# Kernel tuning notes

Hardware: AMD Instinct MI355X
Metric: run time of the kernel (lower is better)

## Reference

```python
import jax, jax.numpy as jnp
import numpy as np

N, C, K, KEIG, B, NG, H = 32768, 128, 5, 128, 64, 512, 4
E = 524288
EPS = 1e-5


def setup_inputs() -> dict:
    key = jax.random.key(0)
    ks = iter(jax.random.split(key, 40))
    def nrm(shape, scale):
        return jax.random.normal(next(ks), shape, jnp.float32) * scale
    s = 1.0 / np.sqrt(C)
    return dict(
        x=nrm((N, C), 1.0),
        U=nrm((N, KEIG), 1.0 / np.sqrt(N)),
        Lambda=jax.random.uniform(next(ks), (KEIG,), jnp.float32, 0.0, 2.0),
        lambda_max=jnp.full((1,), 2.0, jnp.float32),
        w_spa1=nrm((C, C), s), b_spa1=jnp.zeros((C,), jnp.float32),
        w_spa2=nrm((C, C), s), b_spa2=jnp.zeros((C,), jnp.float32),
        w_spe1=nrm((C, C), s), b_spe1=jnp.zeros((C,), jnp.float32),
        w_spe2=nrm((C, C), s), b_spe2=jnp.zeros((C,), jnp.float32),
        cheb_w=nrm((K, C, C), s), cheb_b=jnp.zeros((C,), jnp.float32),
        gamma=jnp.ones((1,), jnp.float32),
        w_proj=nrm((C, C), s),
        w_qkv=nrm((C, 3 * C), s), b_qkv=jnp.zeros((3 * C,), jnp.float32),
        w_out=nrm((C, C), s), b_out=jnp.zeros((C,), jnp.float32),
        mlp_w1=nrm((C, 2 * C), s), mlp_b1=jnp.zeros((2 * C,), jnp.float32),
        mlp_w2=nrm((2 * C, C), 1.0 / np.sqrt(2 * C)), mlp_b2=jnp.zeros((C,), jnp.float32),
        bn1_w=jnp.ones((C,), jnp.float32), bn1_b=jnp.zeros((C,), jnp.float32),
        bn2_w=jnp.ones((C,), jnp.float32), bn2_b=jnp.zeros((C,), jnp.float32),
        bn3_w=jnp.ones((C,), jnp.float32), bn3_b=jnp.zeros((C,), jnp.float32),
        edge_index=jax.random.randint(next(ks), (2, E), 0, N, jnp.int64) if jax.config.jax_enable_x64 else jax.random.randint(next(ks), (2, E), 0, N, jnp.int32),
        batch=jnp.repeat(jnp.arange(B), NG),  # 64 graphs of 512 nodes each
    )


def _mlp2(h, w1, b1, w2, b2):
    return jnp.maximum(h @ w1 + b1, 0.0) @ w2 + b2


def _bn(h, w, b):
    # train-mode BatchNorm1d over node dim (biased variance), GPSConv default norm
    mu = h.mean(0)
    var = jnp.mean((h - mu) ** 2, 0)
    return (h - mu) * jax.lax.rsqrt(var + EPS) * w + b


def _cheb(x, src, dst, lam, Ws, bias):
    # L_hat = (2/lambda_max) * (I - D^{-1/2} A D^{-1/2}) - I ; sym normalization
    deg = jax.ops.segment_sum(jnp.ones_like(src, x.dtype), src, num_segments=N)
    dis = jnp.where(deg > 0, 1.0 / jnp.sqrt(deg), 0.0)
    w = dis[src] * dis[dst]  # [E]
    scale = 2.0 / lam
    def lhat(v):
        agg = jax.ops.segment_sum(w[:, None] * v[src], dst, num_segments=N)
        return (scale - 1.0) * v - scale * agg
    Tx0 = x
    out = Tx0 @ Ws[0]
    Tx1 = lhat(Tx0)
    out = out + Tx1 @ Ws[1]
    for k in range(2, K):
        Tx2 = 2.0 * lhat(Tx1) - Tx0
        out = out + Tx2 @ Ws[k]
        Tx0, Tx1 = Tx1, Tx2
    return out + bias


def _mha(xd, w_qkv, b_qkv, w_out, b_out):
    Bq, n, _ = xd.shape
    dh = C // H
    qkv = xd @ w_qkv + b_qkv  # [B,n,3C]
    q, k, v = jnp.split(qkv, 3, axis=-1)
    heads = lambda t: t.reshape(Bq, n, H, dh).transpose(0, 2, 1, 3)
    q, k, v = heads(q), heads(k), heads(v)
    a = jax.nn.softmax(jnp.einsum('bhqd,bhkd->bhqk', q, k) / np.sqrt(dh), axis=-1)
    o = jnp.einsum('bhqk,bhkd->bhqd', a, v).transpose(0, 2, 1, 3).reshape(Bq, n, C)
    return o @ w_out + b_out


def reference(x, U, Lambda, lambda_max,
              w_spa1, b_spa1, w_spa2, b_spa2,
              w_spe1, b_spe1, w_spe2, b_spe2,
              cheb_w, cheb_b, gamma, w_proj,
              w_qkv, b_qkv, w_out, b_out,
              mlp_w1, mlp_b1, mlp_w2, mlp_b2,
              bn1_w, bn1_b, bn2_w, bn2_b, bn3_w, bn3_b,
              edge_index, batch):
    src, dst = edge_index[0], edge_index[1]
    lam = lambda_max[0]
    # ---- SpectralLocalNN (GPSConv local conv branch) ----
    x_sp = _mlp2(x, w_spa1, b_spa1, w_spa2, b_spa2)
    out_local = _cheb(x_sp, src, dst, lam, cheb_w, cheb_b)
    x_spec = _mlp2(x, w_spe1, b_spe1, w_spe2, b_spe2)
    h_proj = x_spec @ w_proj
    s_lam = jnp.exp(-gamma[0] * Lambda ** 2)  # [k_eig]
    out_spectral = U @ (s_lam[:, None] * (U.T @ h_proj))
    h1 = _bn(out_local + out_spectral + x, bn1_w, bn1_b)
    # ---- global attention branch (equal-size graphs -> dense reshape) ----
    xd = x.reshape(B, NG, C)
    h2 = _mha(xd, w_qkv, b_qkv, w_out, b_out).reshape(N, C)
    h2 = _bn(h2 + x, bn2_w, bn2_b)
    # ---- combine + MLP ----
    out = h1 + h2
    out = out + _mlp2(out, mlp_w1, mlp_b1, mlp_w2, mlp_b2)
    return _bn(out, bn3_w, bn3_b)
```

## Files before the change

### kernel.cpp

```cpp
#include <hip/hip_runtime.h>

typedef short bf16x8 __attribute__((ext_vector_type(8)));
typedef short bf16x4 __attribute__((ext_vector_type(4)));
typedef float f32x4 __attribute__((ext_vector_type(4)));

#define DEVI __device__ __forceinline__

constexpr int N   = 32768;
constexpr int C   = 128;
constexpr int E   = 524288;
constexpr float EPSV = 1e-5f;
constexpr int UT_BLOCKS = 128;
constexpr int HB  = 64;
constexpr int EPB = E / HB;
constexpr float QSCALE = 0.17677669529663687f * 1.4426950408889634f;

DEVI float bf2f(ushort u){ return __uint_as_float(((uint)u) << 16); }
DEVI ushort f2bf(float f){
  uint u = __float_as_uint(f);
  return (ushort)((u + 0x7fffu + ((u >> 16) & 1u)) >> 16);
}
DEVI uint cvtpk(float lo, float hi){
  uint r;
  asm("v_cvt_pk_bf16_f32 %0, %1, %2" : "=v"(r) : "v"(lo), "v"(hi));
  return r;
}
DEVI float fexp2(float x){
  float r;
  asm("v_exp_f32 %0, %1" : "=v"(r) : "v"(x));
  return r;
}
DEVI float sane(float v){ if (!(v == v)) return 0.f; return fminf(fmaxf(v, -1e30f), 1e30f); }
DEVI bool mode_fp32(const uint* lmraw){ return (lmraw[0] & 0xffffu) == 0u; }

constexpr int CSZ[28] = {128,1,16384,128,16384,128,16384,128,16384,128,81920,128,
                         1,16384,49152,384,16384,128,32768,256,32768,128,
                         128,128,128,128,128,128};
constexpr int COF[28] = {0,128,192,16576,16704,33088,33216,49600,49728,66112,
                         66240,148160,148288,148352,164736,213888,214272,230656,
                         230784,263552,263808,296576,296704,296832,296960,297088,
                         297216,297344};
constexpr int CAN_SMALL_TOTAL = 297472;

constexpr int WT_SPA1 = 0;
constexpr int WT_SPA2 = 16384;
constexpr int WT_SPE1 = 32768;
constexpr int WT_SPE2 = 49152;
constexpr int WT_PROJ = 65536;
constexpr int WT_CHEB = 81920;
constexpr int WT_QKV  = 163840;
constexpr int WT_WOUT = 212992;
constexpr int WT_MLP1 = 229376;
constexpr int WT_MLP2 = 262144;
constexpr int WT_TOTAL = 294912;

struct CvtArgs { const void* src[28]; };

DEVI ushort cvt_elem(const void* p, int j, bool f32){
  return f32 ? f2bf(((const float*)p)[j]) : ((const ushort*)p)[j];
}

__global__ __launch_bounds__(256) void prep_all(CvtArgs a,
    const void* __restrict__ xs, const void* __restrict__ Us,
    ushort* __restrict__ canx, ushort* __restrict__ canu,
    ushort* __restrict__ cs, ushort* __restrict__ wt,
    int* __restrict__ zp, const uint* __restrict__ lmraw)
{
  bool f32 = mode_fp32(lmraw);
  int b = blockIdx.x, tid = threadIdx.x;
  if (b < 8192) {
    size_t e = ((size_t)b * 256 + tid) * 4;
    bool isU = e >= (size_t)N * C;
    size_t off = isU ? e - (size_t)N * C : e;
    const void* src = isU ? Us : xs;
    ushort* dst = isU ? canu : canx;
    ushort4 o;
    if (f32) {
      float4 v = *(const float4*)((const float*)src + off);
      o.x = f2bf(v.x); o.y = f2bf(v.y); o.z = f2bf(v.z); o.w = f2bf(v.w);
    } else {
      o = *(const ushort4*)((const ushort*)src + off);
    }
    *(ushort4*)(dst + off) = o;
  } else if (b < 9354) {
    int idx = (b - 8192) * 256 + tid;
    #pragma unroll 1
    for (int s = 0; s < 28; s++) {
      if (idx < CSZ[s]) { cs[COF[s] + idx] = cvt_elem(a.src[s], idx, f32); return; }
      idx -= CSZ[s];
    }
  } else if (b < 10506) {
    int i = (b - 9354) * 256 + tid;
    if (i < 81920) {
      int m = i >> 14, r = i & 16383; int k = r >> 7, n = r & 127;
      const void* src = m==0?a.src[2] : m==1?a.src[4] : m==2?a.src[6] : m==3?a.src[8] : a.src[13];
      wt[m*16384 + n*128 + k] = cvt_elem(src, r, f32);
    } else if (i < 163840) {
      int j = i - 81920; int m = j >> 14, r = j & 16383; int k = r >> 7, n = r & 127;
      wt[WT_CHEB + n*640 + m*128 + k] = cvt_elem(a.src[10], j, f32);
    } else if (i < 212992) {
      int j = i - 163840; int k = j / 384, n = j % 384;
      wt[WT_QKV + n*128 + k] = cvt_elem(a.src[14], j, f32);
    } else if (i < 229376) {
      int j = i - 212992; int k = j >> 7, n = j & 127;
      wt[WT_WOUT + n*128 + k] = cvt_elem(a.src[16], j, f32);
    } else if (i < 262144) {
      int j = i - 229376; int k = j >> 8, n = j & 255;
      wt[WT_MLP1 + n*128 + k] = cvt_elem(a.src[18], j, f32);
    } else if (i < WT_TOTAL) {
      int j = i - 262144; int k = j >> 7, n = j & 127;
      wt[WT_MLP2 + n*256 + k] = cvt_elem(a.src[20], j, f32);
    }
  } else {
    int i = (b - 10506) * 256 + tid;
    if (i < 6144) zp[i] = 0;
  }
}

__global__ __launch_bounds__(1024) void hist_lds(const int* __restrict__ ei,
    int* __restrict__ cei, ushort* __restrict__ part)
{
  __shared__ uint hist[N / 2];
  int t = threadIdx.x;
  int b = blockIdx.x;
  bool i64 = ((ei[1] | ei[3] | ei[5] | ei[7]) == 0);
  size_t j0 = (size_t)b * EPB;
  #pragma unroll
  for (int i = t; i < N / 2; i += 1024) hist[i] = 0u;
  __syncthreads();
  for (int k = t; k < EPB; k += 1024) {
    size_t j = j0 + k;
    int v = (i64 ? ei[2 * j] : ei[j]) & (N - 1);
    cei[j] = v;
    atomicAdd(&hist[v >> 1], 1u << ((v & 1) * 16));
  }
  __syncthreads();
  uint* po = (uint*)(part + (size_t)b * N);
  for (int i = t; i < N / 2; i += 1024) po[i] = hist[i];
}

__global__ __launch_bounds__(256) void reduce_cnt(const ushort* __restrict__ part,
    int* __restrict__ cdt, float* __restrict__ dis)
{
  int d = blockIdx.x * 256 + threadIdx.x;
  int s = 0, tt = 0;
  #pragma unroll 8
  for (int b = 0; b < HB; b++) s  += part[(size_t)b * N + d];
  #pragma unroll 8
  for (int b = 0; b < HB; b++) tt += part[(size_t)(HB + b) * N + d];
  cdt[d] = tt;
  dis[d] = s > 0 ? rsqrtf((float)s) : 0.f;
}

__global__ __launch_bounds__(1024) void scan_kernel(const int* __restrict__ cnt,
                                                    int* __restrict__ row_ptr)
{
  __shared__ int sums[1024];
  int t = threadIdx.x;
  int loc[32]; int s = 0;
  int base = t * 32;
  #pragma unroll
  for (int i = 0; i < 32; i++) { loc[i] = s; s += cnt[base + i]; }
  sums[t] = s;
  __syncthreads();
  for (int off = 1; off < 1024; off <<= 1) {
    int v = (t >= off) ? sums[t - off] : 0;
    __syncthreads();
    sums[t] += v;
    __syncthreads();
  }
  int pre = (t == 0) ? 0 : sums[t - 1];
  #pragma unroll
  for (int i = 0; i < 32; i++) row_ptr[base + i] = pre + loc[i];
}

__global__ __launch_bounds__(256) void off_kernel(const int* __restrict__ rp,
    const ushort* __restrict__ part, int* __restrict__ off2)
{
  int d = blockIdx.x * 256 + threadIdx.x;
  int run = rp[d];
  #pragma unroll 8
  for (int b = 0; b < HB; b++) {
    off2[(size_t)b * N + d] = run;
    run += part[(size_t)(HB + b) * N + d];
  }
}

__global__ __launch_bounds__(1024) void edge_scatter(const int* __restrict__ cei,
    const int* __restrict__ off2, const float* __restrict__ dis,
    int2* __restrict__ ep)
{
  __shared__ int base[N];
  int t = threadIdx.x;
  int b = blockIdx.x;
  for (int i = t; i < N; i += 1024) base[i] = off2[(size_t)b * N + i];
  __syncthreads();
  size_t e0 = (size_t)b * EPB;
  for (int k = t; k < EPB; k += 1024) {
    size_t e = e0 + k;
    int s = cei[e], d = cei[e + E];
    int slot = atomicAdd(&base[d], 1);
    int2 v; v.x = s; v.y = __float_as_int(dis[s] * dis[d]);
    ep[slot] = v;
  }
}

template<int K, int COLS, bool RELU, int OMODE, bool BIAS, bool RES, int ASTR, int OSTR, bool QSC, bool STATS>
__global__ __launch_bounds__(256) void gemm_lds(
    const ushort* __restrict__ A, const ushort* __restrict__ WT,
    const ushort* __restrict__ bias, const ushort* __restrict__ res,
    void* __restrict__ outp, float* __restrict__ gstats)
{
  constexpr int NSEG = COLS / 128;
  constexpr int NKC = K / 128;
  constexpr int BP = 136;
  __shared__ ushort Bs[128 * BP];
  __shared__ float ls[STATS ? 256 : 1];
  int tid = threadIdx.x;
  int lane = tid & 63, wave = tid >> 6;
  int quad = lane >> 4, l16 = lane & 15;
  int seg = (NSEG > 1) ? (blockIdx.x % NSEG) : 0;
  int rb  = (NSEG > 1) ? (blockIdx.x / NSEG) : blockIdx.x;
  int row0 = rb * 64 + wave * 16;
  const ushort* wseg = WT + (size_t)(seg * 128) * K;

  f32x4 acc[8];
  #pragma unroll
  for (int nt = 0; nt < 8; nt++) acc[nt] = (f32x4){0.f, 0.f, 0.f, 0.f};

  for (int kc = 0; kc < NKC; kc++) {
    if (kc) __syncthreads();
    #pragma unroll
    for (int i = tid; i < 2048; i += 256) {
      int col = i >> 4, ko = (i & 15) * 8;
      *(bf16x8*)&Bs[col * BP + ko] =
          *(const bf16x8*)(wseg + (size_t)col * K + kc * 128 + ko);
    }
    __syncthreads();
    bf16x8 a[4];
    const ushort* ap = A + (size_t)(row0 + l16) * ASTR + kc * 128 + quad * 8;
    #pragma unroll
    for (int kk = 0; kk < 4; kk++) a[kk] = *(const bf16x8*)(ap + kk * 32);
    #pragma unroll
    for (int kk = 0; kk < 4; kk++) {
      #pragma unroll
      for (int nt = 0; nt < 8; nt++) {
        bf16x8 b = *(const bf16x8*)(&Bs[(nt * 16 + l16) * BP + kk * 32 + quad * 8]);
        acc[nt] = __builtin_amdgcn_mfma_f32_16x16x32_bf16(a[kk], b, acc[nt], 0, 0, 0);
      }
    }
  }

  if (STATS) {
    if (tid < 256) ls[tid] = 0.f;
    __syncthreads();
  }

  #pragma unroll
  for (int nt = 0; nt < 8; nt++) {
    int col = seg * 128 + nt * 16 + l16;
    float bv = 0.f;
    if (BIAS) bv = bf2f(bias[col]);
    float cs_ = 0.f, cs2 = 0.f;
    #pragma unroll
    for (int r = 0; r < 4; r++) {
      int row = row0 + quad * 4 + r;
      size_t oi = (size_t)row * OSTR + col;
      float v = acc[nt][r] + bv;
      if (RES) v += bf2f(res[(size_t)row * COLS + col]);
      if (RELU) v = fmaxf(v, 0.f);
      if (QSC && col < 128) v *= QSCALE;
      float nv;
      if (OMODE == 0)      { ((ushort*)outp)[oi] = f2bf(v); nv = v; }
      else if (OMODE == 1) { ((float*)outp)[oi] = v; nv = v; }
      else                 { float* fo = (float*)outp + oi; nv = *fo + v; *fo = nv; }
      if (STATS) { float sv = sane(nv); cs_ += sv; cs2 += sv * sv; }
    }
    if (STATS) { atomicAdd(&ls[col], cs_); atomicAdd(&ls[128 + col], cs2); }
  }

  if (STATS) {
    __syncthreads();
    float* gs = gstats + (blockIdx.x & 7) * 256;
    if (tid < 128) {
      atomicAdd(&gs[tid], ls[tid]);
      atomicAdd(&gs[128 + tid], ls[128 + tid]);
    }
  }
}

__global__ __launch_bounds__(256) void gemm_qkv(
    const ushort* __restrict__ A, const ushort* __restrict__ WT,
    const ushort* __restrict__ bias, ushort* __restrict__ outp)
{
  constexpr int BP = 136;
  __shared__ ushort Bs[128 * BP];
  int tid = threadIdx.x;
  int lane = tid & 63, wave = tid >> 6;
  int quad = lane >> 4, l16 = lane & 15;
  int row0 = blockIdx.x * 64 + wave * 16;
  bf16x8 a[4];
  {
    const ushort* ap = A + (size_t)(row0 + l16) * 128 + quad * 8;
    #pragma unroll
    for (int kk = 0; kk < 4; kk++) a[kk] = *(const bf16x8*)(ap + kk * 32);
  }

  #pragma unroll 1
  for (int seg = 0; seg < 3; seg++) {
    if (seg) __syncthreads();
    for (int i = tid; i < 2048; i += 256) {
      int col = i >> 4, ko = (i & 15) * 8;
      *(bf16x8*)&Bs[col * BP + ko] =
          *(const bf16x8*)(WT + (size_t)(seg * 128 + col) * 128 + ko);
    }
    __syncthreads();
    f32x4 acc[8];
    #pragma unroll
    for (int nt = 0; nt < 8; nt++) acc[nt] = (f32x4){0.f, 0.f, 0.f, 0.f};
    #pragma unroll
    for (int kk = 0; kk < 4; kk++)
      #pragma unroll
      for (int nt = 0; nt < 8; nt++) {
        bf16x8 b = *(const bf16x8*)(&Bs[(nt * 16 + l16) * BP + kk * 32 + quad * 8]);
        acc[nt] = __builtin_amdgcn_mfma_f32_16x16x32_bf16(a[kk], b, acc[nt], 0, 0, 0);
      }
    #pragma unroll
    for (int nt = 0; nt < 8; nt++) {
      int col = seg * 128 + nt * 16 + l16;
      float bv = bf2f(bias[col]);
      #pragma unroll
      for (int r = 0; r < 4; r++) {
        float v = acc[nt][r] + bv;
        if (seg == 0) v *= QSCALE;
        outp[(size_t)(row0 + quad * 4 + r) * 384 + col] = f2bf(v);
      }
    }
  }
}

template<bool THIRD, int OSTR>
__global__ __launch_bounds__(256) void gemm_chain(
    const ushort* __restrict__ A,
    const ushort* __restrict__ W1, const ushort* __restrict__ B1,
    const ushort* __restrict__ W2, const ushort* __restrict__ B2,
    const ushort* __restrict__ W3,
    ushort* __restrict__ outp)
{
  constexpr int BP = 136;
  __shared__ ushort Bs[128 * BP];
  __shared__ ushort Ts[64 * BP];
  int tid = threadIdx.x;
  int lane = tid & 63, wave = tid >> 6;
  int quad = lane >> 4, l16 = lane & 15;
  int row0 = blockIdx.x * 64 + wave * 16;
  int lw = wave * 16;

  for (int i = tid; i < 2048; i += 256) {
    int col = i >> 4, ko = (i & 15) * 8;
    *(bf16x8*)&Bs[col * BP + ko] = *(const bf16x8*)(W1 + (size_t)col * 128 + ko);
  }
  __syncthreads();
  bf16x8 a[4];
  {
    const ushort* ap = A + (size_t)(row0 + l16) * 128 + quad * 8;
    #pragma unroll
    for (int kk = 0; kk < 4; kk++) a[kk] = *(const bf16x8*)(ap + kk * 32);
  }
  f32x4 acc[8];
  #pragma unroll
  for (int nt = 0; nt < 8; nt++) acc[nt] = (f32x4){0.f, 0.f, 0.f, 0.f};
  #pragma unroll
  for (int kk = 0; kk < 4; kk++)
    #pragma unroll
    for (int nt = 0; nt < 8; nt++) {
      bf16x8 b = *(const bf16x8*)(&Bs[(nt * 16 + l16) * BP + kk * 32 + quad * 8]);
      acc[nt] = __builtin_amdgcn_mfma_f32_16x16x32_bf16(a[kk], b, acc[nt], 0, 0, 0);
    }
  #pragma unroll
  for (int nt = 0; nt < 8; nt++) {
    int col = nt * 16 + l16;
    float bv = bf2f(B1[col]);
    #pragma unroll
    for (int r = 0; r < 4; r++)
      Ts[(lw + quad * 4 + r) * BP + col] = f2bf(fmaxf(acc[nt][r] + bv, 0.f));
  }
  __syncthreads();

  for (int i = tid; i < 2048; i += 256) {
    int col = i >> 4, ko = (i & 15) * 8;
    *(bf16x8*)&Bs[col * BP + ko] = *(const bf16x8*)(W2 + (size_t)col * 128 + ko);
  }
  #pragma unroll
  for (int kk = 0; kk < 4; kk++)
    a[kk] = *(const bf16x8*)(&Ts[(lw + l16) * BP + kk * 32 + quad * 8]);
  __syncthreads();
  #pragma unroll
  for (int nt = 0; nt < 8; nt++) acc[nt] = (f32x4){0.f, 0.f, 0.f, 0.f};
  #pragma unroll
  for (int kk = 0; kk < 4; kk++)
    #pragma unroll
    for (int nt = 0; nt < 8; nt++) {
      bf16x8 b = *(const bf16x8*)(&Bs[(nt * 16 + l16) * BP + kk * 32 + quad * 8]);
      acc[nt] = __builtin_amdgcn_mfma_f32_16x16x32_bf16(a[kk], b, acc[nt], 0, 0, 0);
    }

  if (!THIRD) {
    #pragma unroll
    for (int nt = 0; nt < 8; nt++) {
      int col = nt * 16 + l16;
      float bv = bf2f(B2[col]);
      #pragma unroll
      for (int r = 0; r < 4; r++)
        outp[(size_t)(row0 + quad * 4 + r) * OSTR + col] = f2bf(acc[nt][r] + bv);
    }
    return;
  }

  __syncthreads();
  #pragma unroll
  for (int nt = 0; nt < 8; nt++) {
    int col = nt * 16 + l16;
    float bv = bf2f(B2[col]);
    #pragma unroll
    for (int r = 0; r < 4; r++)
      Ts[(lw + quad * 4 + r) * BP + col] = f2bf(acc[nt][r] + bv);
  }
  __syncthreads();
  for (int i = tid; i < 2048; i += 256) {
    int col = i >> 4, ko = (i & 15) * 8;
    *(bf16x8*)&Bs[col * BP + ko] = *(const bf16x8*)(W3 + (size_t)col * 128 + ko);
  }
  #pragma unroll
  for (int kk = 0; kk < 4; kk++)
    a[kk] = *(const bf16x8*)(&Ts[(lw + l16) * BP + kk * 32 + quad * 8]);
  __syncthreads();
  #pragma unroll
  for (int nt = 0; nt < 8; nt++) acc[nt] = (f32x4){0.f, 0.f, 0.f, 0.f};
  #pragma unroll
  for (int kk = 0; kk < 4; kk++)
    #pragma unroll
    for (int nt = 0; nt < 8; nt++) {
      bf16x8 b = *(const bf16x8*)(&Bs[(nt * 16 + l16) * BP + kk * 32 + quad * 8]);
      acc[nt] = __builtin_amdgcn_mfma_f32_16x16x32_bf16(a[kk], b, acc[nt], 0, 0, 0);
    }
  #pragma unroll
  for (int nt = 0; nt < 8; nt++) {
    int col = nt * 16 + l16;
    #pragma unroll
    for (int r = 0; r < 4; r++)
      outp[(size_t)(row0 + quad * 4 + r) * OSTR + col] = f2bf(acc[nt][r]);
  }
}

__global__ __launch_bounds__(256) void gemm_mlp(
    const ushort* __restrict__ A,
    const ushort* __restrict__ W1, const ushort* __restrict__ B1,
    const ushort* __restrict__ W2, const ushort* __restrict__ B2,
    const ushort* __restrict__ res, float* __restrict__ outp,
    float* __restrict__ gstats)
{
  constexpr int BP = 136;
  constexpr int HP = 264;
  __shared__ ushort Bs[128 * BP];
  __shared__ ushort Hs[64 * HP];
  __shared__ float ls[256];
  int tid = threadIdx.x;
  int lane = tid & 63, wave = tid >> 6;
  int quad = lane >> 4, l16 = lane & 15;
  int row0 = blockIdx.x * 64 + wave * 16;
  int lw = wave * 16;

  bf16x8 a[4];
  {
    const ushort* ap = A + (size_t)(row0 + l16) * 128 + quad * 8;
    #pragma unroll
    for (int kk = 0; kk < 4; kk++) a[kk] = *(const bf16x8*)(ap + kk * 32);
  }

  for (int seg = 0; seg < 2; seg++) {
    if (seg) __syncthreads();
    for (int i = tid; i < 2048; i += 256) {
      int col = i >> 4, ko = (i & 15) * 8;
      *(bf16x8*)&Bs[col * BP + ko] =
          *(const bf16x8*)(W1 + (size_t)(seg * 128 + col) * 128 + ko);
    }
    __syncthreads();
    f32x4 acc[8];
    #pragma unroll
    for (int nt = 0; nt < 8; nt++) acc[nt] = (f32x4){0.f, 0.f, 0.f, 0.f};
    #pragma unroll
    for (int kk = 0; kk < 4; kk++)
      #pragma unroll
      for (int nt = 0; nt < 8; nt++) {
        bf16x8 b = *(const bf16x8*)(&Bs[(nt * 16 + l16) * BP + kk * 32 + quad * 8]);
        acc[nt] = __builtin_amdgcn_mfma_f32_16x16x32_bf16(a[kk], b, acc[nt], 0, 0, 0);
      }
    #pragma unroll
    for (int nt = 0; nt < 8; nt++) {
      int col = seg * 128 + nt * 16 + l16;
      float bv = bf2f(B1[col]);
      #pragma unroll
      for (int r = 0; r < 4; r++)
        Hs[(lw + quad * 4 + r) * HP + col] = f2bf(fmaxf(acc[nt][r] + bv, 0.f));
    }
  }
  __syncthreads();
  if (tid < 256) ls[tid] = 0.f;

  f32x4 acc2[8];
  #pragma unroll
  for (int nt = 0; nt < 8; nt++) acc2[nt] = (f32x4){0.f, 0.f, 0.f, 0.f};
  for (int kc = 0; kc < 2; kc++) {
    if (kc) __syncthreads();
    for (int i = tid; i < 2048; i += 256) {
      int col = i >> 4, ko = (i & 15) * 8;
      *(bf16x8*)&Bs[col * BP + ko] =
          *(const bf16x8*)(W2 + (size_t)col * 256 + kc * 128 + ko);
    }
    bf16x8 a2[4];
    #pragma unroll
    for (int kk = 0; kk < 4; kk++)
      a2[kk] = *(const bf16x8*)(&Hs[(lw + l16) * HP + kc * 128 + kk * 32 + quad * 8]);
    __syncthreads();
    #pragma unroll
    for (int kk = 0; kk < 4; kk++)
      #pragma unroll
      for (int nt = 0; nt < 8; nt++) {
        bf16x8 b = *(const bf16x8*)(&Bs[(nt * 16 + l16) * BP + kk * 32 + quad * 8]);
        acc2[nt] = __builtin_amdgcn_mfma_f32_16x16x32_bf16(a2[kk], b, acc2[nt], 0, 0, 0);
      }
  }

  #pragma unroll
  for (int nt = 0; nt < 8; nt++) {
    int col = nt * 16 + l16;
    float bv = bf2f(B2[col]);
    float cs_ = 0.f, cs2 = 0.f;
    #pragma unroll
    for (int r = 0; r < 4; r++) {
      int row = row0 + quad * 4 + r;
      float v = acc2[nt][r] + bv + bf2f(res[(size_t)row * 128 + col]);
      outp[(size_t)row * 128 + col] = v;
      float sv = sane(v); cs_ += sv; cs2 += sv * sv;
    }
    atomicAdd(&ls[col], cs_); atomicAdd(&ls[128 + col], cs2);
  }
  __syncthreads();
  float* gs = gstats + (blockIdx.x & 7) * 256;
  if (tid < 128) {
    atomicAdd(&gs[tid], ls[tid]);
    atomicAdd(&gs[128 + tid], ls[128 + tid]);
  }
}

__global__ __launch_bounds__(256) void spmm_cheb(
    const int* __restrict__ row_ptr, const int2* __restrict__ ep,
    const ushort* __restrict__ v,
    const ushort* __restrict__ txprev, ushort* __restrict__ txout,
    const ushort* __restrict__ lambda_max, int first, int str)
{
  int wave = threadIdx.x >> 6, lane = threadIdx.x & 63;
  int sub = lane >> 4, l16 = lane & 15;
  int d = blockIdx.x * 4 + wave;
  float lm = bf2f(lambda_max[0]);
  float scale = 2.f / lm;
  if (!(scale == scale) || fabsf(scale) > 1e6f) scale = 1.f;
  int beg = row_ptr[d];
  int end = (d == N - 1) ? E : row_ptr[d + 1];
  float acc[8] = {0.f,0.f,0.f,0.f,0.f,0.f,0.f,0.f};
  int j0 = beg + sub;
  int2 eA = ep[j0 < end ? j0 : 0];
  int2 eB = ep[(j0 + 4) < end ? (j0 + 4) : 0];
  bf16x8 vA = *(const bf16x8*)(v + (size_t)(eA.x & (N - 1)) * str + l16 * 8);
  for (int jb = beg; jb < end; jb += 4) {
    int jc = jb + 8 + sub;
    int2 eC = ep[jc < end ? jc : 0];
    bf16x8 vB = *(const bf16x8*)(v + (size_t)(eB.x & (N - 1)) * str + l16 * 8);
    bool ok = (jb + sub) < end;
    float w = ok ? __int_as_float(eA.y) : 0.f;
    #pragma unroll
    for (int i = 0; i < 8; i++) acc[i] += w * bf2f((ushort)vA[i]);
    eA = eB; eB = eC; vA = vB;
  }
  #pragma unroll
  for (int i = 0; i < 8; i++) {
    acc[i] += __shfl_xor(acc[i], 16);
    acc[i] += __shfl_xor(acc[i], 32);
  }
  if (sub == 0) {
    bf16x8 vd = *(const bf16x8*)(v + (size_t)d * str + l16 * 8);
    bf16x8 tp;
    if (!first) tp = *(const bf16x8*)(txprev + (size_t)d * str + l16 * 8);
    bf16x8 ov;
    #pragma unroll
    for (int i = 0; i < 8; i++) {
      float r = (scale - 1.f) * bf2f((ushort)vd[i]) - scale * acc[i];
      if (!first) r = 2.f * r - bf2f((ushort)tp[i]);
      ov[i] = (short)f2bf(r);
    }
    *(bf16x8*)(txout + (size_t)d * str + l16 * 8) = ov;
  }
}

__global__ __launch_bounds__(256) void ut_mfma(const ushort* __restrict__ U,
    const ushort* __restrict__ hp, float* __restrict__ parts)
{
  constexpr int RP = 40;
  __shared__ ushort Ut[128 * RP];
  __shared__ ushort Ht[128 * RP];
  int t = threadIdx.x;
  int lane = t & 63, wave = t >> 6;
  int quad = lane >> 4, l16 = lane & 15;

  f32x4 acc[2][8];
  #pragma unroll
  for (int a = 0; a < 2; a++)
    #pragma unroll
    for (int ct = 0; ct < 8; ct++) acc[a][ct] = (f32x4){0.f, 0.f, 0.f, 0.f};

  for (int ch = 0; ch < 8; ch++) {
    int n0 = blockIdx.x * 256 + ch * 32;
    __syncthreads();
    for (int i = t; i < 2048; i += 256) {
      int r2 = i >> 7, c = i & 127;
      uint u0 = U [(size_t)(n0 + r2 * 2) * 128 + c];
      uint u1 = U [(size_t)(n0 + r2 * 2 + 1) * 128 + c];
      *(uint*)&Ut[c * RP + r2 * 2] = (u0 & 0xffffu) | (u1 << 16);
      uint h0 = hp[(size_t)(n0 + r2 * 2) * 128 + c];
      uint h1 = hp[(size_t)(n0 + r2 * 2 + 1) * 128 + c];
      *(uint*)&Ht[c * RP + r2 * 2] = (h0 & 0xffffu) | (h1 << 16);
    }
    __syncthreads();
    bf16x8 bfr[8];
    #pragma unroll
    for (int ct = 0; ct < 8; ct++)
      bfr[ct] = *(const bf16x8*)(&Ht[(ct * 16 + l16) * RP + quad * 8]);
    #pragma unroll
    for (int a = 0; a < 2; a++) {
      int kt = wave * 2 + a;
      bf16x8 af = *(const bf16x8*)(&Ut[(kt * 16 + l16) * RP + quad * 8]);
      #pragma unroll
      for (int ct = 0; ct < 8; ct++)
        acc[a][ct] = __builtin_amdgcn_mfma_f32_16x16x32_bf16(af, bfr[ct], acc[a][ct], 0, 0, 0);
    }
  }

  float* po = parts + (size_t)blockIdx.x * 16384;
  #pragma unroll
  for (int a = 0; a < 2; a++) {
    int kt = wave * 2 + a;
    #pragma unroll
    for (int ct = 0; ct < 8; ct++)
      #pragma unroll
      for (int r = 0; r < 4; r++)
        po[(kt * 16 + quad * 4 + r) * 128 + ct * 16 + l16] = acc[a][ct][r];
  }
}

__global__ __launch_bounds__(256) void reduce_mt(const float* __restrict__ parts,
    const ushort* __restrict__ Lambda, const ushort* __restrict__ gamma,
    ushort* __restrict__ MT)
{
  int e = blockIdx.x * 256 + threadIdx.x;
  int keig = e >> 7, c = e & 127;
  float s = 0.f;
  for (int p = 0; p < UT_BLOCKS; p++) s += parts[(size_t)p * 16384 + e];
  float g = bf2f(gamma[0]);
  float lam = bf2f(Lambda[keig]);
  float sl = __expf(-g * lam * lam);
  MT[c * 128 + keig] = f2bf(sl * s);
}

__global__ __launch_bounds__(256) void bn_apply(const float* __restrict__ h,
    const float* __restrict__ st, const ushort* __restrict__ gw,
    const ushort* __restrict__ gb, const ushort* __restrict__ add,
    void* __restrict__ out, const uint* __restrict__ lmraw, int final_out)
{
  __shared__ float sk[128], sb[128];
  int tid = threadIdx.x;
  if (tid < 128) {
    float s = 0.f, s2 = 0.f;
    #pragma unroll
    for (int rr = 0; rr < 8; rr++) {
      s  += st[rr * 256 + tid];
      s2 += st[rr * 256 + 128 + tid];
    }
    float mu  = s * (1.f / 32768.f);
    float var = fmaxf(s2 * (1.f / 32768.f) - mu * mu, 0.f);
    float k = rsqrtf(var + EPSV) * bf2f(gw[tid]);
    sk[tid] = k;
    sb[tid] = bf2f(gb[tid]) - mu * k;
  }
  __syncthreads();
  size_t e = ((size_t)blockIdx.x * 256 + tid) * 4;
  int c0 = (int)(e & 127);
  float4 hv = *(const float4*)(h + e);
  float xv[4] = {sane(hv.x), sane(hv.y), sane(hv.z), sane(hv.w)};
  float addv[4] = {0.f, 0.f, 0.f, 0.f};
  if (add) {
    ushort4 av = *(const ushort4*)(add + e);
    addv[0] = bf2f(av.x); addv[1] = bf2f(av.y);
    addv[2] = bf2f(av.z); addv[3] = bf2f(av.w);
  }
  float r[4];
  #pragma unroll
  for (int j = 0; j < 4; j++) {
    int c = c0 + j;
    r[j] = xv[j] * sk[c] + sb[c] + addv[j];
  }
  if (final_out && mode_fp32(lmraw)) {
    float4 o4; o4.x = r[0]; o4.y = r[1]; o4.z = r[2]; o4.w = r[3];
    *(float4*)((float*)out + e) = o4;
  } else {
    ushort4 o;
    o.x = f2bf(r[0]); o.y = f2bf(r[1]); o.z = f2bf(r[2]); o.w = f2bf(r[3]);
    *(ushort4*)((ushort*)out + e) = o;
  }
}

__global__ __launch_bounds__(256) void bn12_apply(
    const float* __restrict__ ha, const float* __restrict__ hb,
    const float* __restrict__ st1, const float* __restrict__ st2,
    const ushort* __restrict__ w1, const ushort* __restrict__ b1,
    const ushort* __restrict__ w2, const ushort* __restrict__ b2,
    ushort* __restrict__ comb)
{
  __shared__ float k1[128], o1[128], k2[128], o2[128];
  int tid = threadIdx.x;
  if (tid < 128) {
    float s = 0.f, s2 = 0.f, t = 0.f, t2 = 0.f;
    #pragma unroll
    for (int rr = 0; rr < 8; rr++) {
      s  += st1[rr * 256 + tid];  s2 += st1[rr * 256 + 128 + tid];
      t  += st2[rr * 256 + tid];  t2 += st2[rr * 256 + 128 + tid];
    }
    float mu  = s * (1.f / 32768.f);
    float var = fmaxf(s2 * (1.f / 32768.f) - mu * mu, 0.f);
    float k = rsqrtf(var + EPSV) * bf2f(w1[tid]);
    k1[tid] = k; o1[tid] = bf2f(b1[tid]) - mu * k;
    mu  = t * (1.f / 32768.f);
    var = fmaxf(t2 * (1.f / 32768.f) - mu * mu, 0.f);
    k = rsqrtf(var + EPSV) * bf2f(w2[tid]);
    k2[tid] = k; o2[tid] = bf2f(b2[tid]) - mu * k;
  }
  __syncthreads();
  size_t e = ((size_t)blockIdx.x * 256 + tid) * 4;
  int c0 = (int)(e & 127);
  float4 av = *(const float4*)(ha + e);
  float4 bv = *(const float4*)(hb + e);
  float xa[4] = {sane(av.x), sane(av.y), sane(av.z), sane(av.w)};
  float xb[4] = {sane(bv.x), sane(bv.y), sane(bv.z), sane(bv.w)};
  ushort4 o;
  ushort r_[4];
  #pragma unroll
  for (int j = 0; j < 4; j++) {
    int c = c0 + j;
    float h1v = bf2f(f2bf(xa[j] * k1[c] + o1[c]));
    r_[j] = f2bf(xb[j] * k2[c] + o2[c] + h1v);
  }
  o.x = r_[0]; o.y = r_[1]; o.z = r_[2]; o.w = r_[3];
  *(ushort4*)(comb + e) = o;
}

__global__ __launch_bounds__(512) void attn_mfma(const ushort* __restrict__ qkv,
                                                 ushort* __restrict__ attn)
{
  constexpr int VP = 516;
  constexpr int KP = 40;
  __shared__ ushort Kt[512 * KP];
  __shared__ ushort Vt[32 * VP];
  int b = blockIdx.x;
  int g = b >> 3, hh = (b >> 1) & 3, half = b & 1;
  int lane = threadIdx.x & 63, wave = threadIdx.x >> 6;
  int quad = lane >> 4, l16 = lane & 15;
  const ushort* base = qkv + (size_t)g * 512 * 384;

  for (int i = threadIdx.x; i < 512 * 4; i += 512) {
    int key = i >> 2, c8 = (i & 3) * 8;
    *(bf16x8*)&Kt[key * KP + c8] =
        *(const bf16x8*)(base + (size_t)key * 384 + 128 + hh * 32 + c8);
  }
  for (int i = threadIdx.x; i < 256 * 8; i += 512) {
    int kp = i >> 3, d4 = (i & 7) * 4;
    const ushort* va = base + (size_t)(2 * kp) * 384 + 256 + hh * 32 + d4;
    ushort4 a = *(const ushort4*)va;
    ushort4 c = *(const ushort4*)(va + 384);
    *(uint*)&Vt[(d4 + 0) * VP + 2 * kp] = (uint)a.x | ((uint)c.x << 16);
    *(uint*)&Vt[(d4 + 1) * VP + 2 * kp] = (uint)a.y | ((uint)c.y << 16);
    *(uint*)&Vt[(d4 + 2) * VP + 2 * kp] = (uint)a.z | ((uint)c.z << 16);
    *(uint*)&Vt[(d4 + 3) * VP + 2 * kp] = (uint)a.w | ((uint)c.w << 16);
  }
  __syncthreads();

  int q0 = half * 256 + wave * 32;
  bf16x8 qf[2];
  #pragma unroll
  for (int i = 0; i < 2; i++)
    qf[i] = *(const bf16x8*)(base + (size_t)(q0 + i * 16 + l16) * 384 + hh * 32 + quad * 8);

  f32x4 O[2][2];
  #pragma unroll
  for (int dt = 0; dt < 2; dt++)
    #pragma unroll
    for (int i = 0; i < 2; i++) O[dt][i] = (f32x4){0.f, 0.f, 0.f, 0.f};
  float lsum[2] = {0.f, 0.f};

  union PU { uint u[4]; bf16x8 v; };
  union VU { uint2 a[2]; bf16x8 v; };

  for (int kt2 = 0; kt2 < 16; kt2++) {
    int k0 = kt2 * 32;
    bf16x8 kfA = *(const bf16x8*)&Kt[(k0 + l16) * KP + quad * 8];
    bf16x8 kfB = *(const bf16x8*)&Kt[(k0 + 16 + l16) * KP + quad * 8];
    PU pw[2];
    #pragma unroll
    for (int i = 0; i < 2; i++) {
      f32x4 sA = __builtin_amdgcn_mfma_f32_16x16x32_bf16(kfA, qf[i], (f32x4){0.f,0.f,0.f,0.f}, 0, 0, 0);
      f32x4 sB = __builtin_amdgcn_mfma_f32_16x16x32_bf16(kfB, qf[i], (f32x4){0.f,0.f,0.f,0.f}, 0, 0, 0);
      float p0 = fexp2(fminf(sA[0], 86.5f));
      float p1 = fexp2(fminf(sA[1], 86.5f));
      float p2 = fexp2(fminf(sA[2], 86.5f));
      float p3 = fexp2(fminf(sA[3], 86.5f));
      float p4 = fexp2(fminf(sB[0], 86.5f));
      float p5 = fexp2(fminf(sB[1], 86.5f));
      float p6 = fexp2(fminf(sB[2], 86.5f));
      float p7 = fexp2(fminf(sB[3], 86.5f));
      lsum[i] += ((p0 + p1) + (p2 + p3)) + ((p4 + p5) + (p6 + p7));
      pw[i].u[0] = cvtpk(p0, p1); pw[i].u[1] = cvtpk(p2, p3);
      pw[i].u[2] = cvtpk(p4, p5); pw[i].u[3] = cvtpk(p6, p7);
    }
    #pragma unroll
    for (int dt = 0; dt < 2; dt++) {
      int drow = (dt * 16 + l16) * VP;
      VU vu;
      vu.a[0] = *(const uint2*)&Vt[drow + k0 + quad * 4];
      vu.a[1] = *(const uint2*)&Vt[drow + k0 + 16 + quad * 4];
      #pragma unroll
      for (int i = 0; i < 2; i++)
        O[dt][i] = __builtin_amdgcn_mfma_f32_16x16x32_bf16(vu.v, pw[i].v, O[dt][i], 0, 0, 0);
    }
  }

  #pragma unroll
  for (int i = 0; i < 2; i++) {
    float l = lsum[i];
    l += __shfl_xor(l, 16);
    l += __shfl_xor(l, 32);
    lsum[i] = 1.f / l;
  }

  #pragma unroll
  for (int i = 0; i < 2; i++) {
    size_t node = (size_t)g * 512 + q0 + i * 16 + l16;
    #pragma unroll
    for (int dt = 0; dt < 2; dt++) {
      uint2 o;
      o.x = cvtpk(O[dt][i][0] * lsum[i], O[dt][i][1] * lsum[i]);
      o.y = cvtpk(O[dt][i][2] * lsum[i], O[dt][i][3] * lsum[i]);
      *(uint2*)(attn + node * 128 + hh * 32 + dt * 16 + quad * 4) = o;
    }
  }
}

constexpr size_t KB = 1024;
constexpr size_t MB = 1048576;
constexpr size_t OFF_WT    = 0;
constexpr size_t OFF_CDT   = 576 * KB;
constexpr size_t OFF_RP    = 704 * KB;
constexpr size_t OFF_DIS   = 832 * KB;
constexpr size_t OFF_MT    = 960 * KB;
constexpr size_t OFF_STATS = 1024 * KB;
constexpr size_t OFF_CEI   = 6  * MB;
constexpr size_t OFF_EP    = 10 * MB;
constexpr size_t OFF_CANX  = 14 * MB;
constexpr size_t OFF_CANU  = 22 * MB;
constexpr size_t OFF_CANS  = 30 * MB;
constexpr size_t OFF_F1    = 31 * MB;
constexpr size_t OFF_HPROJ = 39 * MB;
constexpr size_t OFF_TBIG  = 47 * MB;
constexpr size_t OFF_PARTH = OFF_TBIG;
constexpr size_t OFF_OFF2  = OFF_TBIG + 8 * MB;
constexpr size_t OFF_F1B   = 71 * MB;
constexpr size_t OFF_PARTS = 87 * MB;

extern "C" void kernel_launch(void* const* d_in, const int* in_sizes, int n_in,
                              void* d_out, int out_size, void* d_ws, size_t ws_size,
                              hipStream_t stream) {
  (void)in_sizes; (void)n_in; (void)out_size; (void)ws_size;
  const uint* lmraw = (const uint*)d_in[3];
  const int*  ei    = (const int*)d_in[30];

  char* W = (char*)d_ws;
  ushort* wt    = (ushort*)(W + OFF_WT);
  int*    cdt   = (int*)(W + OFF_CDT);
  int*    rp    = (int*)(W + OFF_RP);
  float*  dis   = (float*)(W + OFF_DIS);
  ushort* MT    = (ushort*)(W + OFF_MT);
  float*  stats = (float*)(W + OFF_STATS);
  int*    cei   = (int*)(W + OFF_CEI);
  int2*   ep    = (int2*)(W + OFF_EP);
  ushort* part  = (ushort*)(W + OFF_PARTH);
  int*    off2  = (int*)(W + OFF_OFF2);
  ushort* canx  = (ushort*)(W + OFF_CANX);
  ushort* canu  = (ushort*)(W + OFF_CANU);
  ushort* cs    = (ushort*)(W + OFF_CANS);
  float*  F1    = (float*)(W + OFF_F1);
  float*  F1B   = (float*)(W + OFF_F1B);
  ushort* hproj = (ushort*)(W + OFF_HPROJ);
  ushort* Tbig  = (ushort*)(W + OFF_TBIG);
  ushort* qkvb  = (ushort*)(W + OFF_TBIG);
  float*  parts = (float*)(W + OFF_PARTS);
  ushort* attnb = (ushort*)(W + OFF_PARTS);
  ushort* comb  = (ushort*)(W + OFF_CANX);

  const ushort* cLambda = cs + COF[0];
  const ushort* cLmx    = cs + COF[1];
  const ushort* cBspa1  = cs + COF[3];
  const ushort* cBspa2  = cs + COF[5];
  const ushort* cBspe1  = cs + COF[7];
  const ushort* cBspe2  = cs + COF[9];
  const ushort* cChebB  = cs + COF[11];
  const ushort* cGam    = cs + COF[12];
  const ushort* cBqkv   = cs + COF[15];
  const ushort* cBout   = cs + COF[17];
  const ushort* cMb1    = cs + COF[19];
  const ushort* cMb2    = cs + COF[21];
  const ushort* cBn1w   = cs + COF[22];
  const ushort* cBn1b   = cs + COF[23];
  const ushort* cBn2w   = cs + COF[24];
  const ushort* cBn2b   = cs + COF[25];
  const ushort* cBn3w   = cs + COF[26];
  const ushort* cBn3b   = cs + COF[27];

  const ushort* NUL = nullptr;
  float* NULF = nullptr;

  CvtArgs ca;
  ca.src[0]  = d_in[2];  ca.src[1]  = d_in[3];  ca.src[2]  = d_in[4];
  ca.src[3]  = d_in[5];  ca.src[4]  = d_in[6];  ca.src[5]  = d_in[7];
  ca.src[6]  = d_in[8];  ca.src[7]  = d_in[9];  ca.src[8]  = d_in[10];
  ca.src[9]  = d_in[11]; ca.src[10] = d_in[12]; ca.src[11] = d_in[13];
  ca.src[12] = d_in[14]; ca.src[13] = d_in[15]; ca.src[14] = d_in[16];
  ca.src[15] = d_in[17]; ca.src[16] = d_in[18]; ca.src[17] = d_in[19];
  ca.src[18] = d_in[20]; ca.src[19] = d_in[21]; ca.src[20] = d_in[22];
  ca.src[21] = d_in[23]; ca.src[22] = d_in[24]; ca.src[23] = d_in[25];
  ca.src[24] = d_in[26]; ca.src[25] = d_in[27]; ca.src[26] = d_in[28];
  ca.src[27] = d_in[29];
  prep_all<<<10530, 256, 0, stream>>>(ca, d_in[0], d_in[1], canx, canu, cs, wt,
                                      (int*)(W + OFF_STATS), lmraw);

  hist_lds<<<2 * HB, 1024, 0, stream>>>(ei, cei, part);
  reduce_cnt<<<N / 256, 256, 0, stream>>>(part, cdt, dis);
  scan_kernel<<<1, 1024, 0, stream>>>(cdt, rp);
  off_kernel<<<N / 256, 256, 0, stream>>>(rp, part, off2);
  edge_scatter<<<HB, 1024, 0, stream>>>(cei, off2, dis, ep);

  dim3 g1(512), bb(256);
  gemm_chain<false, 640><<<g1, bb, 0, stream>>>(canx, wt + WT_SPA1, cBspa1,
      wt + WT_SPA2, cBspa2, NUL, Tbig);
  gemm_chain<true, 128><<<g1, bb, 0, stream>>>(canx, wt + WT_SPE1, cBspe1,
      wt + WT_SPE2, cBspe2, wt + WT_PROJ, hproj);

  ut_mfma<<<UT_BLOCKS, 256, 0, stream>>>(canu, hproj, parts);
  reduce_mt<<<64, 256, 0, stream>>>(parts, cLambda, cGam, MT);

  spmm_cheb<<<N / 4, 256, 0, stream>>>(rp, ep, Tbig,       NUL,        Tbig + 128, cLmx, 1, 640);
  spmm_cheb<<<N / 4, 256, 0, stream>>>(rp, ep, Tbig + 128, Tbig,       Tbig + 256, cLmx, 0, 640);
  spmm_cheb<<<N / 4, 256, 0, stream>>>(rp, ep, Tbig + 256, Tbig + 128, Tbig + 384, cLmx, 0, 640);
  spmm_cheb<<<N / 4, 256, 0, stream>>>(rp, ep, Tbig + 384, Tbig + 256, Tbig + 512, cLmx, 0, 640);
  gemm_lds<640,128,false,1,true ,false,640,128,false,false><<<g1, bb, 0, stream>>>(Tbig, wt + WT_CHEB, cChebB, NUL, F1, NULF);

  gemm_lds<128,128,false,2,false,true ,128,128,false,true ><<<g1, bb, 0, stream>>>(canu, MT, NUL, canx, F1, stats);

  gemm_qkv<<<g1, bb, 0, stream>>>(canx, wt + WT_QKV, cBqkv, qkvb);
  attn_mfma<<<512, 512, 0, stream>>>(qkvb, attnb);
  gemm_lds<128,128,false,1,true ,true ,128,128,false,true ><<<g1, bb, 0, stream>>>(attnb, wt + WT_WOUT, cBout, canx, F1B, stats + 2048);

  bn12_apply<<<(N * C) / 1024, 256, 0, stream>>>(F1, F1B, stats, stats + 2048,
      cBn1w, cBn1b, cBn2w, cBn2b, comb);

  gemm_mlp<<<g1, bb, 0, stream>>>(comb, wt + WT_MLP1, cMb1, wt + WT_MLP2, cMb2, comb, F1, stats + 4096);
  bn_apply<<<(N * C) / 1024, 256, 0, stream>>>(F1, stats + 4096, cBn3w, cBn3b, NUL, d_out, lmraw, 1);
}
```

Baseline: 483.0 us.

## Fuse BN1/BN2 combine into MLP GEMM prologue and retune UT/hist block counts

Removes the standalone bn12_apply kernel. The MLP GEMM now computes the BN1/BN2 scale and offset from the stats buffers itself. It builds its bf16 A fragments directly from the two fp32 pre-norm buffers, and recomputes the combined residual in its epilogue. This avoids writing and re-reading the bf16 combined tensor, at the cost of reading the fp32 inputs twice per block and doing extra per-element ALU work. Separately, the U^T·h reduction now uses twice as many blocks with half the rows each, the histogram block count HB is doubled, and a workspace offset is moved to make room.

```diff
diff --git a/kernel.cpp b/kernel.cpp
--- a/kernel.cpp
+++ b/kernel.cpp
@@ -10,8 +10,8 @@
 constexpr int C   = 128;
 constexpr int E   = 524288;
 constexpr float EPSV = 1e-5f;
-constexpr int UT_BLOCKS = 128;
-constexpr int HB  = 64;
+constexpr int UT_BLOCKS = 256;
+constexpr int HB  = 128;
 constexpr int EPB = E / HB;
 constexpr float QSCALE = 0.17677669529663687f * 1.4426950408889634f;
 
@@ -454,28 +454,67 @@
 }
 
 __global__ __launch_bounds__(256) void gemm_mlp(
-    const ushort* __restrict__ A,
+    const float* __restrict__ F1a, const float* __restrict__ F1b,
+    const float* __restrict__ st1, const float* __restrict__ st2,
+    const ushort* __restrict__ bw1, const ushort* __restrict__ bb1,
+    const ushort* __restrict__ bw2, const ushort* __restrict__ bb2,
     const ushort* __restrict__ W1, const ushort* __restrict__ B1,
     const ushort* __restrict__ W2, const ushort* __restrict__ B2,
-    const ushort* __restrict__ res, float* __restrict__ outp,
-    float* __restrict__ gstats)
+    float* __restrict__ outp, float* __restrict__ gstats)
 {
   constexpr int BP = 136;
   constexpr int HP = 264;
   __shared__ ushort Bs[128 * BP];
   __shared__ ushort Hs[64 * HP];
   __shared__ float ls[256];
+  __shared__ float kc1[128], oc1[128], kc2[128], oc2[128];
   int tid = threadIdx.x;
   int lane = tid & 63, wave = tid >> 6;
   int quad = lane >> 4, l16 = lane & 15;
   int row0 = blockIdx.x * 64 + wave * 16;
   int lw = wave * 16;
 
+  if (tid < 128) {
+    float s = 0.f, s2 = 0.f, t = 0.f, t2 = 0.f;
+    #pragma unroll
+    for (int rr = 0; rr < 8; rr++) {
+      s  += st1[rr * 256 + tid];  s2 += st1[rr * 256 + 128 + tid];
+      t  += st2[rr * 256 + tid];  t2 += st2[rr * 256 + 128 + tid];
+    }
+    float mu  = s * (1.f / 32768.f);
+    float var = fmaxf(s2 * (1.f / 32768.f) - mu * mu, 0.f);
+    float k = rsqrtf(var + EPSV) * bf2f(bw1[tid]);
+    kc1[tid] = k; oc1[tid] = bf2f(bb1[tid]) - mu * k;
+    mu  = t * (1.f / 32768.f);
+    var = fmaxf(t2 * (1.f / 32768.f) - mu * mu, 0.f);
+    k = rsqrtf(var + EPSV) * bf2f(bw2[tid]);
+    kc2[tid] = k; oc2[tid] = bf2f(bb2[tid]) - mu * k;
+  }
+  __syncthreads();
+
   bf16x8 a[4];
   {
-    const ushort* ap = A + (size_t)(row0 + l16) * 128 + quad * 8;
-    #pragma unroll
-    for (int kk = 0; kk < 4; kk++) a[kk] = *(const bf16x8*)(ap + kk * 32);
+    int arow = row0 + l16;
+    const float* pa = F1a + (size_t)arow * 128;
+    const float* pb = F1b + (size_t)arow * 128;
+    #pragma unroll
+    for (int kk = 0; kk < 4; kk++) {
+      int c0 = kk * 32 + quad * 8;
+      float4 xa0 = *(const float4*)(pa + c0);
+      float4 xa1 = *(const float4*)(pa + c0 + 4);
+      float4 xb0 = *(const float4*)(pb + c0);
+      float4 xb1 = *(const float4*)(pb + c0 + 4);
+      float xa[8] = {xa0.x, xa0.y, xa0.z, xa0.w, xa1.x, xa1.y, xa1.z, xa1.w};
+      float xb[8] = {xb0.x, xb0.y, xb0.z, xb0.w, xb1.x, xb1.y, xb1.z, xb1.w};
+      bf16x8 frag;
+      #pragma unroll
+      for (int j = 0; j < 8; j++) {
+        int c = c0 + j;
+        float h1v = bf2f(f2bf(sane(xa[j]) * kc1[c] + oc1[c]));
+        frag[j] = (short)f2bf(sane(xb[j]) * kc2[c] + oc2[c] + h1v);
+      }
+      a[kk] = frag;
+    }
   }
 
   for (int seg = 0; seg < 2; seg++) {
@@ -540,7 +579,11 @@
     #pragma unroll
     for (int r = 0; r < 4; r++) {
       int row = row0 + quad * 4 + r;
-      float v = acc2[nt][r] + bv + bf2f(res[(size_t)row * 128 + col]);
+      float xa = sane(F1a[(size_t)row * 128 + col]);
+      float xb = sane(F1b[(size_t)row * 128 + col]);
+      float h1v = bf2f(f2bf(xa * kc1[col] + oc1[col]));
+      ushort cb = f2bf(xb * kc2[col] + oc2[col] + h1v);
+      float v = acc2[nt][r] + bv + bf2f(cb);
       outp[(size_t)row * 128 + col] = v;
       float sv = sane(v); cs_ += sv; cs2 += sv * sv;
     }
@@ -619,8 +662,8 @@
     #pragma unroll
     for (int ct = 0; ct < 8; ct++) acc[a][ct] = (f32x4){0.f, 0.f, 0.f, 0.f};
 
-  for (int ch = 0; ch < 8; ch++) {
-    int n0 = blockIdx.x * 256 + ch * 32;
+  for (int ch = 0; ch < 4; ch++) {
+    int n0 = blockIdx.x * 128 + ch * 32;
     __syncthreads();
     for (int i = t; i < 2048; i += 256) {
       int r2 = i >> 7, c = i & 127;
@@ -717,50 +760,6 @@
     o.x = f2bf(r[0]); o.y = f2bf(r[1]); o.z = f2bf(r[2]); o.w = f2bf(r[3]);
     *(ushort4*)((ushort*)out + e) = o;
   }
-}
-
-__global__ __launch_bounds__(256) void bn12_apply(
-    const float* __restrict__ ha, const float* __restrict__ hb,
-    const float* __restrict__ st1, const float* __restrict__ st2,
-    const ushort* __restrict__ w1, const ushort* __restrict__ b1,
-    const ushort* __restrict__ w2, const ushort* __restrict__ b2,
-    ushort* __restrict__ comb)
-{
-  __shared__ float k1[128], o1[128], k2[128], o2[128];
-  int tid = threadIdx.x;
-  if (tid < 128) {
-    float s = 0.f, s2 = 0.f, t = 0.f, t2 = 0.f;
-    #pragma unroll
-    for (int rr = 0; rr < 8; rr++) {
-      s  += st1[rr * 256 + tid];  s2 += st1[rr * 256 + 128 + tid];
-      t  += st2[rr * 256 + tid];  t2 += st2[rr * 256 + 128 + tid];
-    }
-    float mu  = s * (1.f / 32768.f);
-    float var = fmaxf(s2 * (1.f / 32768.f) - mu * mu, 0.f);
-    float k = rsqrtf(var + EPSV) * bf2f(w1[tid]);
-    k1[tid] = k; o1[tid] = bf2f(b1[tid]) - mu * k;
-    mu  = t * (1.f / 32768.f);
-    var = fmaxf(t2 * (1.f / 32768.f) - mu * mu, 0.f);
-    k = rsqrtf(var + EPSV) * bf2f(w2[tid]);
-    k2[tid] = k; o2[tid] = bf2f(b2[tid]) - mu * k;
-  }
-  __syncthreads();
-  size_t e = ((size_t)blockIdx.x * 256 + tid) * 4;
-  int c0 = (int)(e & 127);
-  float4 av = *(const float4*)(ha + e);
-  float4 bv = *(const float4*)(hb + e);
-  float xa[4] = {sane(av.x), sane(av.y), sane(av.z), sane(av.w)};
-  float xb[4] = {sane(bv.x), sane(bv.y), sane(bv.z), sane(bv.w)};
-  ushort4 o;
-  ushort r_[4];
-  #pragma unroll
-  for (int j = 0; j < 4; j++) {
-    int c = c0 + j;
-    float h1v = bf2f(f2bf(xa[j] * k1[c] + o1[c]));
-    r_[j] = f2bf(xb[j] * k2[c] + o2[c] + h1v);
-  }
-  o.x = r_[0]; o.y = r_[1]; o.z = r_[2]; o.w = r_[3];
-  *(ushort4*)(comb + e) = o;
 }
 
 __global__ __launch_bounds__(512) void attn_mfma(const ushort* __restrict__ qkv,
@@ -880,7 +879,7 @@
 constexpr size_t OFF_HPROJ = 39 * MB;
 constexpr size_t OFF_TBIG  = 47 * MB;
 constexpr size_t OFF_PARTH = OFF_TBIG;
-constexpr size_t OFF_OFF2  = OFF_TBIG + 8 * MB;
+constexpr size_t OFF_OFF2  = OFF_TBIG + 16 * MB;
 constexpr size_t OFF_F1B   = 71 * MB;
 constexpr size_t OFF_PARTS = 87 * MB;
 
@@ -912,7 +911,6 @@
   ushort* qkvb  = (ushort*)(W + OFF_TBIG);
   float*  parts = (float*)(W + OFF_PARTS);
   ushort* attnb = (ushort*)(W + OFF_PARTS);
-  ushort* comb  = (ushort*)(W + OFF_CANX);
 
   const ushort* cLambda = cs + COF[0];
   const ushort* cLmx    = cs + COF[1];
@@ -977,9 +975,8 @@
   attn_mfma<<<512, 512, 0, stream>>>(qkvb, attnb);
   gemm_lds<128,128,false,1,true ,true ,128,128,false,true ><<<g1, bb, 0, stream>>>(attnb, wt + WT_WOUT, cBout, canx, F1B, stats + 2048);
 
-  bn12_apply<<<(N * C) / 1024, 256, 0, stream>>>(F1, F1B, stats, stats + 2048,
-      cBn1w, cBn1b, cBn2w, cBn2b, comb);
-
-  gemm_mlp<<<g1, bb, 0, stream>>>(comb, wt + WT_MLP1, cMb1, wt + WT_MLP2, cMb2, comb, F1, stats + 4096);
+  gemm_mlp<<<g1, bb, 0, stream>>>(F1, F1B, stats, stats + 2048,
+      cBn1w, cBn1b, cBn2w, cBn2b,
+      wt + WT_MLP1, cMb1, wt + WT_MLP2, cMb2, F1, stats + 4096);
   bn_apply<<<(N * C) / 1024, 256, 0, stream>>>(F1, stats + 4096, cBn3w, cBn3b, NUL, d_out, lmraw, 1);
 }
```

Measured after the change: 470.1 us. -2.7%, faster.
